# Optimization experiments

Measured on AMD Instinct MI355X. Metric: run time of the kernel, lower is better.

Reference implementation:

```python
import jax, jax.numpy as jnp
import numpy as np

H = 16          # nhead
EPS = 1e-5      # LayerNorm eps (torch default)


def _layernorm(x, g, b):
    mu = jnp.mean(x, axis=-1, keepdims=True)
    var = jnp.mean(jnp.square(x - mu), axis=-1, keepdims=True)
    return (x - mu) * jax.lax.rsqrt(var + EPS) * g + b


def setup_inputs() -> dict:
    key = jax.random.key(0)
    ks = jax.random.split(key, 8)
    B, L, D, F = 256, 64, 1024, 4096
    s = 0.02
    return {
        "src": jax.random.normal(ks[0], (B, L, D), jnp.float32),
        "Wq": jax.random.normal(ks[1], (D, D), jnp.float32) * s,
        "bq": jnp.zeros((D,), jnp.float32),
        "Wk": jax.random.normal(ks[2], (D, D), jnp.float32) * s,
        "bk": jnp.zeros((D,), jnp.float32),
        "Wv": jax.random.normal(ks[3], (D, D), jnp.float32) * s,
        "bv": jnp.zeros((D,), jnp.float32),
        "Wo": jax.random.normal(ks[4], (D, D), jnp.float32) * s,
        "bo": jnp.zeros((D,), jnp.float32),
        "rel_bias": jax.random.normal(ks[5], (H, 2 * L - 1), jnp.float32) * s,
        "W1": jax.random.normal(ks[6], (D, F), jnp.float32) * s,
        "b1": jnp.zeros((F,), jnp.float32),
        "W2": jax.random.normal(ks[7], (F, D), jnp.float32) * s,
        "b2": jnp.zeros((D,), jnp.float32),
        "g1": jnp.ones((D,), jnp.float32),
        "be1": jnp.zeros((D,), jnp.float32),
        "g2": jnp.ones((D,), jnp.float32),
        "be2": jnp.zeros((D,), jnp.float32),
    }


def reference(src, Wq, bq, Wk, bk, Wv, bv, Wo, bo, rel_bias,
              W1, b1, W2, b2, g1, be1, g2, be2):
    B, L, D = src.shape
    dh = D // H
    # --- relative multi-head attention ---
    q = (src @ Wq + bq).reshape(B, L, H, dh)
    k = (src @ Wk + bk).reshape(B, L, H, dh)
    v = (src @ Wv + bv).reshape(B, L, H, dh)
    scores = jnp.einsum('bqhd,bkhd->bhqk', q, k) / jnp.sqrt(jnp.float32(dh))
    # relative position bias lookup: index i - j + (L-1) into (H, 2L-1) table
    rel_idx = jnp.arange(L)[:, None] - jnp.arange(L)[None, :] + (L - 1)  # (L,L)
    scores = scores + rel_bias[:, rel_idx]  # broadcast (H,L,L) over batch
    attn = jax.nn.softmax(scores, axis=-1)
    ctx = jnp.einsum('bhqk,bkhd->bqhd', attn, v).reshape(B, L, D)
    attn_out = ctx @ Wo + bo
    # --- residual + LN + FFN + residual + LN (dropout = eval no-op) ---
    x = _layernorm(src + attn_out, g1, be1)
    ff = jax.nn.gelu(x @ W1 + b1) @ W2 + b2
    return _layernorm(x + ff, g2, be2)
```

## Files before the change

kernel.cpp:

```cpp
#include <hip/hip_runtime.h>

typedef __bf16 bf16;
typedef __attribute__((ext_vector_type(8))) __bf16 bf16x8;
typedef __attribute__((ext_vector_type(4))) __bf16 bf16x4;
typedef __attribute__((ext_vector_type(4))) float f32x4;

#define N_TOK 16384
#define DMODEL 1024
#define FDIM 4096
#define NHEAD 16

__device__ __forceinline__ void gload_lds16(const bf16* g, bf16* l) {
  __builtin_amdgcn_global_load_lds(
      (const __attribute__((address_space(1))) void*)g,
      (__attribute__((address_space(3))) void*)l,
      16, 0, 0);
}

__device__ __forceinline__ float gelu_tanh(float x) {
  return 0.5f * x * (1.0f + tanhf(0.7978845608028654f * (x + 0.044715f * x * x * x)));
}

__global__ __launch_bounds__(256) void cvt_copy(const float* __restrict__ x,
                                                bf16* __restrict__ y) {
  size_t i = ((size_t)blockIdx.x * 256 + threadIdx.x) * 8;
  float4 a = *(const float4*)(x + i);
  float4 b = *(const float4*)(x + i + 4);
  bf16x8 o;
  o[0] = (bf16)a.x; o[1] = (bf16)a.y; o[2] = (bf16)a.z; o[3] = (bf16)a.w;
  o[4] = (bf16)b.x; o[5] = (bf16)b.y; o[6] = (bf16)b.z; o[7] = (bf16)b.w;
  *(bf16x8*)(y + i) = o;
}

__global__ void convt(const float* __restrict__ src, bf16* __restrict__ dst,
                      int R, int C) {
  __shared__ float tile[32][33];
  int c0 = blockIdx.x * 32, r0 = blockIdx.y * 32;
  int tx = threadIdx.x, ty = threadIdx.y;
#pragma unroll
  for (int i = 0; i < 4; ++i)
    tile[ty * 4 + i][tx] = src[(size_t)(r0 + ty * 4 + i) * C + c0 + tx];
  __syncthreads();
#pragma unroll
  for (int i = 0; i < 4; ++i)
    dst[(size_t)(c0 + ty * 4 + i) * R + r0 + tx] = (bf16)tile[tx][ty * 4 + i];
}


__device__ __forceinline__ void stage_half(const bf16* g, int ldg, bf16* region,
                                           int wv, int lane) {
#pragma unroll
  for (int j = 0; j < 2; ++j) {
    int c = wv * 2 + j;
    int r = c * 8 + (lane >> 3);
    int col = ((lane & 7) * 8) ^ ((r & 7) * 8);
    gload_lds16(g + (size_t)r * ldg + col, region + c * 512 + lane * 8);
  }
}

__device__ __forceinline__ bf16x8 frag_ld(const bf16* s, int row, int kc) {
  return *(const bf16x8*)(s + row * 64 + (kc ^ ((row & 7) * 8)));
}

template <int RES, int GELU>
__global__ __launch_bounds__(512) void gemm256(
    const bf16* __restrict__ A, const bf16* __restrict__ BT,
    const float* __restrict__ bias, const float* __restrict__ resf,
    const bf16* __restrict__ resb, bf16* __restrict__ C,
    int M, int N, int K) {
  __shared__ alignas(16) bf16 sA[2][256 * 64];
  __shared__ alignas(16) bf16 sB[2][256 * 64];
  const int tid = threadIdx.x;
  const int lane = tid & 63, wv = tid >> 6;
  const int wr = wv >> 2, wc = wv & 3;
  const int r16 = lane & 15, hk = lane >> 4;

  const int nbn = N >> 8;
  const int cpx = gridDim.x >> 3;
  const int swz = ((int)blockIdx.x & 7) * cpx + ((int)blockIdx.x >> 3);
  const int row0 = (swz / nbn) << 8, col0 = (swz % nbn) << 8;

  const bf16* Ab = A + (size_t)row0 * K;
  const bf16* Bb = BT + (size_t)col0 * K;

  f32x4 acc[8][4] = {};
  bf16x8 aF[4][2], bF0[2][2], bF1[2][2];

  stage_half(Ab,                      K, &sA[0][0],        wv, lane);
  stage_half(Ab + 128 * (size_t)K,    K, &sA[0][128 * 64], wv, lane);
  stage_half(Bb,                      K, &sB[0][0],        wv, lane);
  stage_half(Bb + 128 * (size_t)K,    K, &sB[0][128 * 64], wv, lane);
  asm volatile("s_waitcnt vmcnt(0)" ::: "memory");
  __builtin_amdgcn_s_barrier();

  const int nt = K >> 6;
  for (int kt = 0; kt < nt; ++kt) {
    const bf16* sa = &sA[kt & 1][0];
    const bf16* sb = &sB[kt & 1][0];
    bf16* na = &sA[(kt + 1) & 1][0];
    bf16* nb = &sB[(kt + 1) & 1][0];
    const bool pf = (kt + 1 < nt);
    const size_t koff = (size_t)(kt + 1) << 6;

#pragma unroll
    for (int i = 0; i < 4; ++i)
#pragma unroll
      for (int ks = 0; ks < 2; ++ks)
        aF[i][ks] = frag_ld(sa, wr * 128 + i * 16 + r16, ks * 32 + hk * 8);
#pragma unroll
    for (int j = 0; j < 2; ++j)
#pragma unroll
      for (int ks = 0; ks < 2; ++ks)
        bF0[j][ks] = frag_ld(sb, wc * 64 + j * 16 + r16, ks * 32 + hk * 8);
    if (pf) {
      stage_half(Ab + koff,                   K, na,            wv, lane);
      stage_half(Ab + 128 * (size_t)K + koff, K, na + 128 * 64, wv, lane);
    }
    __builtin_amdgcn_s_barrier();
    __builtin_amdgcn_s_setprio(1);
#pragma unroll
    for (int i = 0; i < 4; ++i)
#pragma unroll
      for (int j = 0; j < 2; ++j)
#pragma unroll
        for (int ks = 0; ks < 2; ++ks)
          acc[i][j] = __builtin_amdgcn_mfma_f32_16x16x32_bf16(bF0[j][ks], aF[i][ks], acc[i][j], 0, 0, 0);
    __builtin_amdgcn_s_setprio(0);
    __builtin_amdgcn_s_barrier();

#pragma unroll
    for (int j = 0; j < 2; ++j)
#pragma unroll
      for (int ks = 0; ks < 2; ++ks)
        bF1[j][ks] = frag_ld(sb, wc * 64 + (2 + j) * 16 + r16, ks * 32 + hk * 8);
    if (pf) {
      stage_half(Bb + koff,                   K, nb,            wv, lane);
      stage_half(Bb + 128 * (size_t)K + koff, K, nb + 128 * 64, wv, lane);
    }
    __builtin_amdgcn_s_barrier();
    __builtin_amdgcn_s_setprio(1);
#pragma unroll
    for (int i = 0; i < 4; ++i)
#pragma unroll
      for (int j = 0; j < 2; ++j)
#pragma unroll
        for (int ks = 0; ks < 2; ++ks)
          acc[i][2 + j] = __builtin_amdgcn_mfma_f32_16x16x32_bf16(bF1[j][ks], aF[i][ks], acc[i][2 + j], 0, 0, 0);
    __builtin_amdgcn_s_setprio(0);
    __builtin_amdgcn_s_barrier();

#pragma unroll
    for (int i = 0; i < 4; ++i)
#pragma unroll
      for (int ks = 0; ks < 2; ++ks)
        aF[i][ks] = frag_ld(sa, wr * 128 + (4 + i) * 16 + r16, ks * 32 + hk * 8);
    __builtin_amdgcn_s_barrier();
    __builtin_amdgcn_s_setprio(1);
#pragma unroll
    for (int i = 0; i < 4; ++i)
#pragma unroll
      for (int j = 0; j < 2; ++j)
#pragma unroll
        for (int ks = 0; ks < 2; ++ks)
          acc[4 + i][2 + j] = __builtin_amdgcn_mfma_f32_16x16x32_bf16(bF1[j][ks], aF[i][ks], acc[4 + i][2 + j], 0, 0, 0);
    __builtin_amdgcn_s_setprio(0);
    __builtin_amdgcn_s_barrier();

    __builtin_amdgcn_s_setprio(1);
#pragma unroll
    for (int i = 0; i < 4; ++i)
#pragma unroll
      for (int j = 0; j < 2; ++j)
#pragma unroll
        for (int ks = 0; ks < 2; ++ks)
          acc[4 + i][j] = __builtin_amdgcn_mfma_f32_16x16x32_bf16(bF0[j][ks], aF[i][ks], acc[4 + i][j], 0, 0, 0);
    __builtin_amdgcn_s_setprio(0);
    asm volatile("s_waitcnt vmcnt(0)" ::: "memory");
    __builtin_amdgcn_s_barrier();
  }

#pragma unroll
  for (int m = 0; m < 8; ++m) {
    int row = row0 + wr * 128 + m * 16 + r16;
#pragma unroll
    for (int n = 0; n < 4; ++n) {
      int col = col0 + wc * 64 + n * 16 + hk * 4;
      f32x4 b4 = *(const f32x4*)&bias[col];
      f32x4 v;
#pragma unroll
      for (int r = 0; r < 4; ++r) v[r] = acc[m][n][r] + b4[r];
      if (RES == 1) {
        f32x4 rr = *(const f32x4*)&resf[(size_t)row * N + col];
#pragma unroll
        for (int r = 0; r < 4; ++r) v[r] += rr[r];
      }
      if (RES == 2) {
        bf16x4 rb = *(const bf16x4*)&resb[(size_t)row * N + col];
#pragma unroll
        for (int r = 0; r < 4; ++r) v[r] += (float)rb[r];
      }
      bf16x4 o;
#pragma unroll
      for (int r = 0; r < 4; ++r) {
        float x = v[r];
        if (GELU) x = gelu_tanh(x);
        o[r] = (bf16)x;
      }
      *(bf16x4*)&C[(size_t)row * N + col] = o;
    }
  }
}

__global__ __launch_bounds__(256) void attn_k(
    const bf16* q, const bf16* __restrict__ k,
    const bf16* __restrict__ v, const float* __restrict__ rel,
    bf16* ctx) {
  __shared__ alignas(16) bf16 lQ[64 * 64];
  __shared__ alignas(16) bf16 lK[64 * 64];
  __shared__ alignas(16) bf16 lVt[64 * 64];
  __shared__ alignas(16) bf16 lP[4][16 * 64];
  __shared__ float lrel[128];

  const int bh = blockIdx.x;
  const int b = bh >> 4, h = bh & 15;
  const int tid = threadIdx.x;
  const size_t base = (size_t)(b * 64) * DMODEL + h * 64;

#pragma unroll
  for (int i = 0; i < 2; ++i) {
    int j = (tid >> 3) + i * 32;
    int d0 = (tid & 7) * 8;
    *(bf16x8*)&lQ[j * 64 + d0] = *(const bf16x8*)(q + base + (size_t)j * DMODEL + d0);
    *(bf16x8*)&lK[j * 64 + d0] = *(const bf16x8*)(k + base + (size_t)j * DMODEL + d0);
    bf16x8 vvv = *(const bf16x8*)(v + base + (size_t)j * DMODEL + d0);
#pragma unroll
    for (int u = 0; u < 8; ++u) lVt[(d0 + u) * 64 + j] = vvv[u];
  }
  if (tid < 127) lrel[tid] = rel[h * 127 + tid];
  __syncthreads();

  const int lane = tid & 63, w = tid >> 6;
  const int r16 = lane & 15, hk = lane >> 4;

  f32x4 s[4] = {};
#pragma unroll
  for (int dstep = 0; dstep < 2; ++dstep) {
    bf16x8 aq = *(const bf16x8*)&lQ[(w * 16 + r16) * 64 + dstep * 32 + hk * 8];
#pragma unroll
    for (int n = 0; n < 4; ++n) {
      bf16x8 bk_ = *(const bf16x8*)&lK[(n * 16 + r16) * 64 + dstep * 32 + hk * 8];
      s[n] = __builtin_amdgcn_mfma_f32_16x16x32_bf16(aq, bk_, s[n], 0, 0, 0);
    }
  }

  float p[16];
#pragma unroll
  for (int n = 0; n < 4; ++n)
#pragma unroll
    for (int r = 0; r < 4; ++r) {
      int i = w * 16 + hk * 4 + r;
      int j = n * 16 + r16;
      p[n * 4 + r] = s[n][r] * 0.125f + lrel[i - j + 63];
    }
#pragma unroll
  for (int r = 0; r < 4; ++r) {
    float m = fmaxf(fmaxf(p[r], p[4 + r]), fmaxf(p[8 + r], p[12 + r]));
#pragma unroll
    for (int off = 1; off < 16; off <<= 1) m = fmaxf(m, __shfl_xor(m, off));
    float sum = 0.f;
#pragma unroll
    for (int n = 0; n < 4; ++n) {
      p[n * 4 + r] = __expf(p[n * 4 + r] - m);
      sum += p[n * 4 + r];
    }
#pragma unroll
    for (int off = 1; off < 16; off <<= 1) sum += __shfl_xor(sum, off);
    float inv = 1.0f / sum;
#pragma unroll
    for (int n = 0; n < 4; ++n) p[n * 4 + r] *= inv;
  }
#pragma unroll
  for (int n = 0; n < 4; ++n)
#pragma unroll
    for (int r = 0; r < 4; ++r)
      lP[w][(hk * 4 + r) * 64 + n * 16 + r16] = (bf16)p[n * 4 + r];
  __syncthreads();

  f32x4 o[4] = {};
#pragma unroll
  for (int ks = 0; ks < 2; ++ks) {
    bf16x8 ap = *(const bf16x8*)&lP[w][r16 * 64 + ks * 32 + hk * 8];
#pragma unroll
    for (int n = 0; n < 4; ++n) {
      bf16x8 bv_ = *(const bf16x8*)&lVt[(n * 16 + r16) * 64 + ks * 32 + hk * 8];
      o[n] = __builtin_amdgcn_mfma_f32_16x16x32_bf16(ap, bv_, o[n], 0, 0, 0);
    }
  }
#pragma unroll
  for (int n = 0; n < 4; ++n)
#pragma unroll
    for (int r = 0; r < 4; ++r) {
      int trow = b * 64 + w * 16 + hk * 4 + r;
      ctx[(size_t)trow * DMODEL + h * 64 + n * 16 + r16] = (bf16)o[n][r];
    }
}

template <int F32OUT>
__global__ __launch_bounds__(256) void layernorm_k(
    const bf16* __restrict__ x, const float* __restrict__ g,
    const float* __restrict__ be, bf16* __restrict__ ob,
    float* __restrict__ of) {
  int row = blockIdx.x * 4 + (threadIdx.x >> 6);
  int lane = threadIdx.x & 63;
  const bf16* xr = x + (size_t)row * DMODEL + lane * 16;
  bf16x8 v0 = *(const bf16x8*)xr;
  bf16x8 v1 = *(const bf16x8*)(xr + 8);
  float f[16];
#pragma unroll
  for (int j = 0; j < 8; ++j) { f[j] = (float)v0[j]; f[8 + j] = (float)v1[j]; }
  float s = 0.f, sq = 0.f;
#pragma unroll
  for (int j = 0; j < 16; ++j) { s += f[j]; sq += f[j] * f[j]; }
#pragma unroll
  for (int off = 1; off < 64; off <<= 1) {
    s += __shfl_xor(s, off);
    sq += __shfl_xor(sq, off);
  }
  float mean = s * (1.0f / DMODEL);
  float var = sq * (1.0f / DMODEL) - mean * mean;
  float rstd = rsqrtf(var + 1e-5f);
  const float* gp = g + lane * 16;
  const float* bp = be + lane * 16;
  if (F32OUT) {
    float* op = of + (size_t)row * DMODEL + lane * 16;
#pragma unroll
    for (int j = 0; j < 16; ++j)
      op[j] = (f[j] - mean) * rstd * gp[j] + bp[j];
  } else {
    bf16x8 o0, o1;
#pragma unroll
    for (int j = 0; j < 8; ++j) {
      o0[j] = (bf16)((f[j] - mean) * rstd * gp[j] + bp[j]);
      o1[j] = (bf16)((f[8 + j] - mean) * rstd * gp[8 + j] + bp[8 + j]);
    }
    bf16* op = ob + (size_t)row * DMODEL + lane * 16;
    *(bf16x8*)op = o0;
    *(bf16x8*)(op + 8) = o1;
  }
}

extern "C" void kernel_launch(void* const* d_in, const int* in_sizes, int n_in,
                              void* d_out, int out_size, void* d_ws, size_t ws_size,
                              hipStream_t stream) {
  (void)in_sizes; (void)n_in; (void)out_size; (void)ws_size;
  const float* src = (const float*)d_in[0];
  const float* Wq  = (const float*)d_in[1];
  const float* bq  = (const float*)d_in[2];
  const float* Wk  = (const float*)d_in[3];
  const float* bk  = (const float*)d_in[4];
  const float* Wv  = (const float*)d_in[5];
  const float* bv  = (const float*)d_in[6];
  const float* Wo  = (const float*)d_in[7];
  const float* bo  = (const float*)d_in[8];
  const float* rel = (const float*)d_in[9];
  const float* W1  = (const float*)d_in[10];
  const float* b1  = (const float*)d_in[11];
  const float* W2  = (const float*)d_in[12];
  const float* b2  = (const float*)d_in[13];
  const float* g1  = (const float*)d_in[14];
  const float* be1 = (const float*)d_in[15];
  const float* g2  = (const float*)d_in[16];
  const float* be2 = (const float*)d_in[17];

  char* ws = (char*)d_ws;
  const size_t MiB = 1ull << 20;
  bf16* srcb = (bf16*)(ws + 0 * MiB);
  bf16* qb   = (bf16*)(ws + 32 * MiB);
  bf16* WqT  = (bf16*)(ws + 64 * MiB);
  bf16* WkT  = (bf16*)(ws + 66 * MiB);
  bf16* WvT  = (bf16*)(ws + 68 * MiB);
  bf16* WoT  = (bf16*)(ws + 70 * MiB);
  bf16* W1T  = (bf16*)(ws + 72 * MiB);
  bf16* W2T  = (bf16*)(ws + 80 * MiB);
  bf16* hbuf = (bf16*)(ws + 0 * MiB);
  float* lnout = (float*)(ws + 0 * MiB);
  bf16* kb = (bf16*)d_out;
  bf16* vb = (bf16*)((char*)d_out + 32 * MiB);
  bf16* y1 = kb;
  bf16* xb = vb;
  bf16* y2 = kb;

  cvt_copy<<<(N_TOK * DMODEL) / 2048, 256, 0, stream>>>(src, srcb);
  dim3 tb(32, 8);
  convt<<<dim3(32, 32), tb, 0, stream>>>(Wq, WqT, 1024, 1024);
  convt<<<dim3(32, 32), tb, 0, stream>>>(Wk, WkT, 1024, 1024);
  convt<<<dim3(32, 32), tb, 0, stream>>>(Wv, WvT, 1024, 1024);
  convt<<<dim3(32, 32), tb, 0, stream>>>(Wo, WoT, 1024, 1024);
  convt<<<dim3(128, 32), tb, 0, stream>>>(W1, W1T, 1024, 4096);
  convt<<<dim3(32, 128), tb, 0, stream>>>(W2, W2T, 4096, 1024);

  const int gQKV = (N_TOK / 256) * (DMODEL / 256);
  gemm256<0, 0><<<gQKV, 512, 0, stream>>>(srcb, WqT, bq, nullptr, nullptr, qb, N_TOK, DMODEL, DMODEL);
  gemm256<0, 0><<<gQKV, 512, 0, stream>>>(srcb, WkT, bk, nullptr, nullptr, kb, N_TOK, DMODEL, DMODEL);
  gemm256<0, 0><<<gQKV, 512, 0, stream>>>(srcb, WvT, bv, nullptr, nullptr, vb, N_TOK, DMODEL, DMODEL);

  attn_k<<<256 * NHEAD, 256, 0, stream>>>(qb, kb, vb, rel, qb);

  gemm256<1, 0><<<gQKV, 512, 0, stream>>>(qb, WoT, bo, src, nullptr, y1, N_TOK, DMODEL, DMODEL);
  layernorm_k<0><<<N_TOK / 4, 256, 0, stream>>>(y1, g1, be1, xb, nullptr);

  const int CH = 8192;
  const int gF1 = (CH / 256) * (FDIM / 256);
  const int gF2 = (CH / 256) * (DMODEL / 256);
  for (int c = 0; c < 2; ++c) {
    const bf16* xc = xb + (size_t)c * CH * DMODEL;
    bf16* yc = y2 + (size_t)c * CH * DMODEL;
    gemm256<0, 1><<<gF1, 512, 0, stream>>>(xc, W1T, b1, nullptr, nullptr, hbuf, CH, FDIM, DMODEL);
    gemm256<2, 0><<<gF2, 512, 0, stream>>>(hbuf, W2T, b2, nullptr, xc, yc, CH, DMODEL, FDIM);
  }
  layernorm_k<1><<<N_TOK / 4, 256, 0, stream>>>(y2, g2, be2, nullptr, lnout);
  hipMemcpyAsync(d_out, lnout, (size_t)N_TOK * DMODEL * 4, hipMemcpyDeviceToDevice, stream);
}
```

Before: 723.9 us.

## Replace GEMM with 4-stage BK=32 pipelined kernel, templated M tile

Rewrites the bf16 GEMM to use a 4-buffer LDS ring with K-step 32. Three tiles are kept in flight via global_load_lds, with vmcnt-based waits and one barrier per step, replacing the double-buffered K=64 loop that had many barriers. The M tile size becomes a template parameter, and the FFN2 GEMM uses 128-row tiles so its grid has more blocks. The aim is to hide global load latency and cut barrier stalls, in exchange for more loop iterations and a new swizzle scheme.

Result: slower. 786.0 us (+8.6%).

```diff
diff --git a/kernel.cpp b/kernel.cpp
--- a/kernel.cpp
+++ b/kernel.cpp
@@ -46,30 +46,20 @@
     dst[(size_t)(c0 + ty * 4 + i) * R + r0 + tx] = (bf16)tile[tx][ty * 4 + i];
 }
 
-
-__device__ __forceinline__ void stage_half(const bf16* g, int ldg, bf16* region,
-                                           int wv, int lane) {
-#pragma unroll
-  for (int j = 0; j < 2; ++j) {
-    int c = wv * 2 + j;
-    int r = c * 8 + (lane >> 3);
-    int col = ((lane & 7) * 8) ^ ((r & 7) * 8);
-    gload_lds16(g + (size_t)r * ldg + col, region + c * 512 + lane * 8);
-  }
-}
-
-__device__ __forceinline__ bf16x8 frag_ld(const bf16* s, int row, int kc) {
-  return *(const bf16x8*)(s + row * 64 + (kc ^ ((row & 7) * 8)));
-}
-
-template <int RES, int GELU>
-__global__ __launch_bounds__(512) void gemm256(
+template <int BM_, int RES, int GELU>
+__global__ __launch_bounds__(512) void gemm_p(
     const bf16* __restrict__ A, const bf16* __restrict__ BT,
     const float* __restrict__ bias, const float* __restrict__ resf,
     const bf16* __restrict__ resb, bf16* __restrict__ C,
     int M, int N, int K) {
-  __shared__ alignas(16) bf16 sA[2][256 * 64];
-  __shared__ alignas(16) bf16 sB[2][256 * 64];
+  constexpr int MF  = BM_ / 32;
+  constexpr int AR  = BM_ / 128;
+  constexpr int LPT = AR + 2;
+  constexpr int ABUF = BM_ * 32;
+  constexpr int BBUF = 256 * 32;
+  __shared__ alignas(16) bf16 sA[4][ABUF];
+  __shared__ alignas(16) bf16 sB[4][BBUF];
+
   const int tid = threadIdx.x;
   const int lane = tid & 63, wv = tid >> 6;
   const int wr = wv >> 2, wc = wv & 3;
@@ -78,110 +68,71 @@
   const int nbn = N >> 8;
   const int cpx = gridDim.x >> 3;
   const int swz = ((int)blockIdx.x & 7) * cpx + ((int)blockIdx.x >> 3);
-  const int row0 = (swz / nbn) << 8, col0 = (swz % nbn) << 8;
+  const int row0 = (swz / nbn) * BM_, col0 = (swz % nbn) << 8;
 
   const bf16* Ab = A + (size_t)row0 * K;
   const bf16* Bb = BT + (size_t)col0 * K;
 
-  f32x4 acc[8][4] = {};
-  bf16x8 aF[4][2], bF0[2][2], bF1[2][2];
-
-  stage_half(Ab,                      K, &sA[0][0],        wv, lane);
-  stage_half(Ab + 128 * (size_t)K,    K, &sA[0][128 * 64], wv, lane);
-  stage_half(Bb,                      K, &sB[0][0],        wv, lane);
-  stage_half(Bb + 128 * (size_t)K,    K, &sB[0][128 * 64], wv, lane);
-  asm volatile("s_waitcnt vmcnt(0)" ::: "memory");
-  __builtin_amdgcn_s_barrier();
-
-  const int nt = K >> 6;
+  const int t4 = tid >> 2;
+  const int scol = ((tid & 3) ^ (t4 & 3)) * 8;
+  const bf16* ga0 = Ab + (size_t)t4 * K + scol;
+  const bf16* ga1 = Ab + (size_t)(128 + t4) * K + scol;
+  const bf16* gb0 = Bb + (size_t)t4 * K + scol;
+  const bf16* gb1 = Bb + (size_t)(128 + t4) * K + scol;
+
+  auto stage = [&](int buf, int kt) {
+    const size_t ko = (size_t)kt << 5;
+    gload_lds16(ga0 + ko, &sA[buf][tid * 8]);
+    if constexpr (AR == 2) gload_lds16(ga1 + ko, &sA[buf][(512 + tid) * 8]);
+    gload_lds16(gb0 + ko, &sB[buf][tid * 8]);
+    gload_lds16(gb1 + ko, &sB[buf][(512 + tid) * 8]);
+  };
+
+  const int swzo = (hk ^ (r16 & 3)) * 8;
+  const int rdA = (wr * (BM_ / 2) + r16) * 32 + swzo;
+  const int rdB = (wc * 64 + r16) * 32 + swzo;
+
+  f32x4 acc[MF][4] = {};
+
+  stage(0, 0);
+  stage(1, 1);
+  stage(2, 2);
+
+  const int nt = K >> 5;
   for (int kt = 0; kt < nt; ++kt) {
-    const bf16* sa = &sA[kt & 1][0];
-    const bf16* sb = &sB[kt & 1][0];
-    bf16* na = &sA[(kt + 1) & 1][0];
-    bf16* nb = &sB[(kt + 1) & 1][0];
-    const bool pf = (kt + 1 < nt);
-    const size_t koff = (size_t)(kt + 1) << 6;
-
-#pragma unroll
-    for (int i = 0; i < 4; ++i)
-#pragma unroll
-      for (int ks = 0; ks < 2; ++ks)
-        aF[i][ks] = frag_ld(sa, wr * 128 + i * 16 + r16, ks * 32 + hk * 8);
-#pragma unroll
-    for (int j = 0; j < 2; ++j)
-#pragma unroll
-      for (int ks = 0; ks < 2; ++ks)
-        bF0[j][ks] = frag_ld(sb, wc * 64 + j * 16 + r16, ks * 32 + hk * 8);
-    if (pf) {
-      stage_half(Ab + koff,                   K, na,            wv, lane);
-      stage_half(Ab + 128 * (size_t)K + koff, K, na + 128 * 64, wv, lane);
+    if (kt + 2 < nt) {
+      if constexpr (LPT == 4) asm volatile("s_waitcnt vmcnt(8)" ::: "memory");
+      else                    asm volatile("s_waitcnt vmcnt(6)" ::: "memory");
+    } else if (kt + 1 < nt) {
+      if constexpr (LPT == 4) asm volatile("s_waitcnt vmcnt(4)" ::: "memory");
+      else                    asm volatile("s_waitcnt vmcnt(3)" ::: "memory");
+    } else {
+      asm volatile("s_waitcnt vmcnt(0)" ::: "memory");
     }
     __builtin_amdgcn_s_barrier();
+
+    if (kt + 3 < nt) stage((kt + 3) & 3, kt + 3);
+
+    const bf16* sa = &sA[kt & 3][0];
+    const bf16* sb = &sB[kt & 3][0];
+    bf16x8 aF[MF], bF[4];
+#pragma unroll
+    for (int n = 0; n < 4; ++n) bF[n] = *(const bf16x8*)(sb + rdB + n * 512);
+#pragma unroll
+    for (int m = 0; m < MF; ++m) aF[m] = *(const bf16x8*)(sa + rdA + m * 512);
+
     __builtin_amdgcn_s_setprio(1);
 #pragma unroll
-    for (int i = 0; i < 4; ++i)
-#pragma unroll
-      for (int j = 0; j < 2; ++j)
-#pragma unroll
-        for (int ks = 0; ks < 2; ++ks)
-          acc[i][j] = __builtin_amdgcn_mfma_f32_16x16x32_bf16(bF0[j][ks], aF[i][ks], acc[i][j], 0, 0, 0);
+    for (int m = 0; m < MF; ++m)
+#pragma unroll
+      for (int n = 0; n < 4; ++n)
+        acc[m][n] = __builtin_amdgcn_mfma_f32_16x16x32_bf16(bF[n], aF[m], acc[m][n], 0, 0, 0);
     __builtin_amdgcn_s_setprio(0);
-    __builtin_amdgcn_s_barrier();
-
-#pragma unroll
-    for (int j = 0; j < 2; ++j)
-#pragma unroll
-      for (int ks = 0; ks < 2; ++ks)
-        bF1[j][ks] = frag_ld(sb, wc * 64 + (2 + j) * 16 + r16, ks * 32 + hk * 8);
-    if (pf) {
-      stage_half(Bb + koff,                   K, nb,            wv, lane);
-      stage_half(Bb + 128 * (size_t)K + koff, K, nb + 128 * 64, wv, lane);
-    }
-    __builtin_amdgcn_s_barrier();
-    __builtin_amdgcn_s_setprio(1);
-#pragma unroll
-    for (int i = 0; i < 4; ++i)
-#pragma unroll
-      for (int j = 0; j < 2; ++j)
-#pragma unroll
-        for (int ks = 0; ks < 2; ++ks)
-          acc[i][2 + j] = __builtin_amdgcn_mfma_f32_16x16x32_bf16(bF1[j][ks], aF[i][ks], acc[i][2 + j], 0, 0, 0);
-    __builtin_amdgcn_s_setprio(0);
-    __builtin_amdgcn_s_barrier();
-
-#pragma unroll
-    for (int i = 0; i < 4; ++i)
-#pragma unroll
-      for (int ks = 0; ks < 2; ++ks)
-        aF[i][ks] = frag_ld(sa, wr * 128 + (4 + i) * 16 + r16, ks * 32 + hk * 8);
-    __builtin_amdgcn_s_barrier();
-    __builtin_amdgcn_s_setprio(1);
-#pragma unroll
-    for (int i = 0; i < 4; ++i)
-#pragma unroll
-      for (int j = 0; j < 2; ++j)
-#pragma unroll
-        for (int ks = 0; ks < 2; ++ks)
-          acc[4 + i][2 + j] = __builtin_amdgcn_mfma_f32_16x16x32_bf16(bF1[j][ks], aF[i][ks], acc[4 + i][2 + j], 0, 0, 0);
-    __builtin_amdgcn_s_setprio(0);
-    __builtin_amdgcn_s_barrier();
-
-    __builtin_amdgcn_s_setprio(1);
-#pragma unroll
-    for (int i = 0; i < 4; ++i)
-#pragma unroll
-      for (int j = 0; j < 2; ++j)
-#pragma unroll
-        for (int ks = 0; ks < 2; ++ks)
-          acc[4 + i][j] = __builtin_amdgcn_mfma_f32_16x16x32_bf16(bF0[j][ks], aF[i][ks], acc[4 + i][j], 0, 0, 0);
-    __builtin_amdgcn_s_setprio(0);
-    asm volatile("s_waitcnt vmcnt(0)" ::: "memory");
-    __builtin_amdgcn_s_barrier();
-  }
-
-#pragma unroll
-  for (int m = 0; m < 8; ++m) {
-    int row = row0 + wr * 128 + m * 16 + r16;
+  }
+
+#pragma unroll
+  for (int m = 0; m < MF; ++m) {
+    int row = row0 + wr * (BM_ / 2) + m * 16 + r16;
 #pragma unroll
     for (int n = 0; n < 4; ++n) {
       int col = col0 + wc * 64 + n * 16 + hk * 4;
@@ -400,23 +351,23 @@
   convt<<<dim3(32, 128), tb, 0, stream>>>(W2, W2T, 4096, 1024);
 
   const int gQKV = (N_TOK / 256) * (DMODEL / 256);
-  gemm256<0, 0><<<gQKV, 512, 0, stream>>>(srcb, WqT, bq, nullptr, nullptr, qb, N_TOK, DMODEL, DMODEL);
-  gemm256<0, 0><<<gQKV, 512, 0, stream>>>(srcb, WkT, bk, nullptr, nullptr, kb, N_TOK, DMODEL, DMODEL);
-  gemm256<0, 0><<<gQKV, 512, 0, stream>>>(srcb, WvT, bv, nullptr, nullptr, vb, N_TOK, DMODEL, DMODEL);
+  gemm_p<256, 0, 0><<<gQKV, 512, 0, stream>>>(srcb, WqT, bq, nullptr, nullptr, qb, N_TOK, DMODEL, DMODEL);
+  gemm_p<256, 0, 0><<<gQKV, 512, 0, stream>>>(srcb, WkT, bk, nullptr, nullptr, kb, N_TOK, DMODEL, DMODEL);
+  gemm_p<256, 0, 0><<<gQKV, 512, 0, stream>>>(srcb, WvT, bv, nullptr, nullptr, vb, N_TOK, DMODEL, DMODEL);
 
   attn_k<<<256 * NHEAD, 256, 0, stream>>>(qb, kb, vb, rel, qb);
 
-  gemm256<1, 0><<<gQKV, 512, 0, stream>>>(qb, WoT, bo, src, nullptr, y1, N_TOK, DMODEL, DMODEL);
+  gemm_p<256, 1, 0><<<gQKV, 512, 0, stream>>>(qb, WoT, bo, src, nullptr, y1, N_TOK, DMODEL, DMODEL);
   layernorm_k<0><<<N_TOK / 4, 256, 0, stream>>>(y1, g1, be1, xb, nullptr);
 
   const int CH = 8192;
   const int gF1 = (CH / 256) * (FDIM / 256);
-  const int gF2 = (CH / 256) * (DMODEL / 256);
+  const int gF2 = (CH / 128) * (DMODEL / 256);
   for (int c = 0; c < 2; ++c) {
     const bf16* xc = xb + (size_t)c * CH * DMODEL;
     bf16* yc = y2 + (size_t)c * CH * DMODEL;
-    gemm256<0, 1><<<gF1, 512, 0, stream>>>(xc, W1T, b1, nullptr, nullptr, hbuf, CH, FDIM, DMODEL);
-    gemm256<2, 0><<<gF2, 512, 0, stream>>>(hbuf, W2T, b2, nullptr, xc, yc, CH, DMODEL, FDIM);
+    gemm_p<256, 0, 1><<<gF1, 512, 0, stream>>>(xc, W1T, b1, nullptr, nullptr, hbuf, CH, FDIM, DMODEL);
+    gemm_p<128, 2, 0><<<gF2, 512, 0, stream>>>(hbuf, W2T, b2, nullptr, xc, yc, CH, DMODEL, FDIM);
   }
   layernorm_k<1><<<N_TOK / 4, 256, 0, stream>>>(y2, g2, be2, nullptr, lnout);
   hipMemcpyAsync(d_out, lnout, (size_t)N_TOK * DMODEL * 4, hipMemcpyDeviceToDevice, stream);
```
